# Optimization experiments

Hardware: AMD Instinct MI355X
Metric: run time of the kernel (lower is better)

## Reference

```python
import jax, jax.numpy as jnp
import numpy as np
from jax import lax

D_MODEL = 512
D_STATE = 16
D_CONV = 4
DT_RANK = 32  # ceil(512/16)


def setup_inputs() -> dict:
    key = jax.random.key(0)
    ks = jax.random.split(key, 8)
    B, L = 4, 2048
    x = jax.random.normal(ks[0], (B, L, D_MODEL), dtype=jnp.float32)
    A_log = jax.random.normal(ks[1], (D_MODEL, D_STATE), dtype=jnp.float32)
    D = jax.random.normal(ks[2], (D_MODEL,), dtype=jnp.float32)
    # torch Linear weight layout: (out_features, in_features)
    x_proj_w = jax.random.normal(ks[3], (DT_RANK + 2 * D_STATE, D_MODEL), dtype=jnp.float32) * (1.0 / np.sqrt(D_MODEL))
    dt_proj_w = jax.random.normal(ks[4], (D_MODEL, DT_RANK), dtype=jnp.float32) * (1.0 / np.sqrt(DT_RANK))
    dt_proj_b = jax.random.normal(ks[5], (D_MODEL,), dtype=jnp.float32) * 0.1
    # depthwise conv: (out_channels, in_channels/groups=1, kernel)
    conv_w = jax.random.normal(ks[6], (D_MODEL, 1, D_CONV), dtype=jnp.float32) * (1.0 / np.sqrt(D_CONV))
    conv_b = jax.random.normal(ks[7], (D_MODEL,), dtype=jnp.float32) * 0.1
    return {"x": x, "A_log": A_log, "D": D, "x_proj_w": x_proj_w,
            "dt_proj_w": dt_proj_w, "dt_proj_b": dt_proj_b,
            "conv_w": conv_w, "conv_b": conv_b}


def reference(x, A_log, D, x_proj_w, dt_proj_w, dt_proj_b, conv_w, conv_b):
    B, L, d_model = x.shape
    # causal depthwise conv1d: torch pads (d_conv-1) both sides then trims right -> left-pad only
    x_t = jnp.transpose(x, (0, 2, 1))  # (B, d, L)
    xc = lax.conv_general_dilated(
        x_t, conv_w, window_strides=(1,), padding=[(D_CONV - 1, 0)],
        feature_group_count=d_model)
    xc = xc + conv_b[None, :, None]
    xc = jnp.transpose(xc, (0, 2, 1))  # (B, L, d)

    x_dbl = xc @ x_proj_w.T  # (B, L, dt_rank + 2*d_state)
    dt = x_dbl[..., :DT_RANK]
    Bm = x_dbl[..., DT_RANK:DT_RANK + D_STATE]       # (B, L, n)
    C = x_dbl[..., DT_RANK + D_STATE:]               # (B, L, n)

    dt = jax.nn.softplus(dt @ dt_proj_w.T + dt_proj_b)  # (B, L, d)
    A = -jnp.exp(A_log.astype(jnp.float32))             # (d, n)
    dA = jnp.exp(jnp.einsum('bld,dn->bldn', dt, A))     # (B, L, d, n)
    dBx = jnp.einsum('bld,bln->bldn', dt * xc, Bm)      # (B, L, d, n)

    def step(h, inputs):
        dA_t, dBx_t, C_t = inputs  # (B,d,n), (B,d,n), (B,n)
        h = dA_t * h + dBx_t
        y_t = jnp.einsum('bdn,bn->bd', h, C_t)
        return h, y_t

    h0 = jnp.zeros((B, d_model, D_STATE), dtype=x.dtype)
    _, ys = lax.scan(step, h0, (jnp.moveaxis(dA, 1, 0), jnp.moveaxis(dBx, 1, 0), jnp.moveaxis(C, 1, 0)))
    y = jnp.moveaxis(ys, 0, 1)  # (B, L, d)
    return y + xc * D[None, None, :]
```

## Files before the change

kernel.cpp:

```cpp
#include <hip/hip_runtime.h>
#include <stdint.h>

#define L_SEQ   2048
#define NBATCH  4
#define DM      512
#define DS      16
#define DR      32
#define NBDN    32768
#define NCH     64
#define CL      32
#define LOG2E   1.4426950408889634f

#define WS_DX    0
#define WS_XDBL  4194304
#define WS_WXT   4718592
#define WS_WDTT  4751360
#define WS_A2    4767744
#define WS_DTSUM 4775936
#define WS_S     4907008

__device__ __forceinline__ uint32_t bf16_rne_hi(float v) {
    uint32_t u = __float_as_uint(v);
    u += 0x7FFF + ((u >> 16) & 1);
    return u & 0xFFFF0000u;
}
__device__ __forceinline__ float bf_lo(uint32_t u) { return __uint_as_float(u << 16); }
__device__ __forceinline__ float bf_hi(uint32_t u) { return __uint_as_float(u & 0xFFFF0000u); }

__global__ void __launch_bounds__(256) k_prep(
        const float* __restrict__ Wx, const float* __restrict__ Wdt,
        const float* __restrict__ A_log, float* __restrict__ WxT,
        float* __restrict__ WdtT, float* __restrict__ A2) {
    int idx = blockIdx.x * 256 + threadIdx.x;
    if (idx < DM * 64) {
        int dd = idx >> 6, j = idx & 63;
        WxT[idx] = Wx[j * DM + dd];
    }
    if (idx < DR * DM) {
        int r = idx >> 9, dd = idx & 511;
        WdtT[idx] = Wdt[dd * DR + r];
    }
    if (idx < DM * DS)
        A2[idx] = -__expf(A_log[idx]) * LOG2E;
}

__global__ void __launch_bounds__(256) k_front(
        const float* __restrict__ x, const float* __restrict__ convw,
        const float* __restrict__ convb, const float* __restrict__ WxT,
        const float* __restrict__ WdtT, const float* __restrict__ dtb,
        uint32_t* __restrict__ dx, float* __restrict__ xdbl) {
    __shared__ float xcs[8][512];
    __shared__ float pt[8][8][64];
    __shared__ float xds[8][64];
    int t  = threadIdx.x;
    int r0 = blockIdx.x * 8;
    int b  = r0 >> 11, l0 = r0 & (L_SEQ - 1);
    int dq = t & 127, half = t >> 7;

    {
        const float4* wp = (const float4*)convw;
        float4 w0 = wp[dq * 4 + 0], w1 = wp[dq * 4 + 1];
        float4 w2 = wp[dq * 4 + 2], w3 = wp[dq * 4 + 3];
        float4 bias = ((const float4*)convb)[dq];
        #pragma unroll
        for (int i = 0; i < 4; ++i) {
            int row = half * 4 + i;
            int l   = l0 + row;
            const float* xr = x + ((size_t)(b * L_SEQ + l)) * DM + dq * 4;
            float4 acc = bias;
            float4 xv = *(const float4*)xr;
            acc.x = fmaf(xv.x, w0.w, acc.x); acc.y = fmaf(xv.y, w1.w, acc.y);
            acc.z = fmaf(xv.z, w2.w, acc.z); acc.w = fmaf(xv.w, w3.w, acc.w);
            if (l >= 1) {
                xv = *(const float4*)(xr - DM);
                acc.x = fmaf(xv.x, w0.z, acc.x); acc.y = fmaf(xv.y, w1.z, acc.y);
                acc.z = fmaf(xv.z, w2.z, acc.z); acc.w = fmaf(xv.w, w3.z, acc.w);
            }
            if (l >= 2) {
                xv = *(const float4*)(xr - 2 * DM);
                acc.x = fmaf(xv.x, w0.y, acc.x); acc.y = fmaf(xv.y, w1.y, acc.y);
                acc.z = fmaf(xv.z, w2.y, acc.z); acc.w = fmaf(xv.w, w3.y, acc.w);
            }
            if (l >= 3) {
                xv = *(const float4*)(xr - 3 * DM);
                acc.x = fmaf(xv.x, w0.x, acc.x); acc.y = fmaf(xv.y, w1.x, acc.y);
                acc.z = fmaf(xv.z, w2.x, acc.z); acc.w = fmaf(xv.w, w3.x, acc.w);
            }
            *(float4*)(&xcs[row][dq * 4]) = acc;
        }
    }
    __syncthreads();

    {
        int ks = t >> 5;
        int jp = t & 31;
        int k0 = ks * 64;
        float accA[8], accB[8];
        #pragma unroll
        for (int ri = 0; ri < 8; ++ri) { accA[ri] = 0.f; accB[ri] = 0.f; }
        const float2* wp2 = (const float2*)WxT;
        for (int k4 = 0; k4 < 16; ++k4) {
            float4 xr[8];
            #pragma unroll
            for (int ri = 0; ri < 8; ++ri)
                xr[ri] = *(const float4*)(&xcs[ri][k0 + k4 * 4]);
            #pragma unroll
            for (int kk = 0; kk < 4; ++kk) {
                float2 w2 = wp2[(size_t)(k0 + k4 * 4 + kk) * 32 + jp];
                #pragma unroll
                for (int ri = 0; ri < 8; ++ri) {
                    float xv = ((const float*)&xr[ri])[kk];
                    accA[ri] = fmaf(xv, w2.x, accA[ri]);
                    accB[ri] = fmaf(xv, w2.y, accB[ri]);
                }
            }
        }
        #pragma unroll
        for (int ri = 0; ri < 8; ++ri)
            *(float2*)(&pt[ks][ri][jp * 2]) = make_float2(accA[ri], accB[ri]);
    }
    __syncthreads();

    #pragma unroll
    for (int o = t; o < 512; o += 256) {
        int row = o >> 6, j2 = o & 63;
        float s = ((pt[0][row][j2] + pt[1][row][j2]) + (pt[2][row][j2] + pt[3][row][j2]))
                + ((pt[4][row][j2] + pt[5][row][j2]) + (pt[6][row][j2] + pt[7][row][j2]));
        xds[row][j2] = s;
        xdbl[(size_t)(r0 + row) * 64 + j2] = s;
    }
    __syncthreads();

    {
        float4 bias = ((const float4*)dtb)[dq];
        float4 z0 = bias, z1 = bias, z2 = bias, z3 = bias;
        for (int r = 0; r < DR; ++r) {
            float4 w4 = *(const float4*)(WdtT + r * DM + dq * 4);
            float x0 = xds[half * 4 + 0][r];
            float x1 = xds[half * 4 + 1][r];
            float x2 = xds[half * 4 + 2][r];
            float x3 = xds[half * 4 + 3][r];
            z0.x = fmaf(x0, w4.x, z0.x); z0.y = fmaf(x0, w4.y, z0.y);
            z0.z = fmaf(x0, w4.z, z0.z); z0.w = fmaf(x0, w4.w, z0.w);
            z1.x = fmaf(x1, w4.x, z1.x); z1.y = fmaf(x1, w4.y, z1.y);
            z1.z = fmaf(x1, w4.z, z1.z); z1.w = fmaf(x1, w4.w, z1.w);
            z2.x = fmaf(x2, w4.x, z2.x); z2.y = fmaf(x2, w4.y, z2.y);
            z2.z = fmaf(x2, w4.z, z2.z); z2.w = fmaf(x2, w4.w, z2.w);
            z3.x = fmaf(x3, w4.x, z3.x); z3.y = fmaf(x3, w4.y, z3.y);
            z3.z = fmaf(x3, w4.z, z3.z); z3.w = fmaf(x3, w4.w, z3.w);
        }
        float4 zz[4] = {z0, z1, z2, z3};
        #pragma unroll
        for (int i = 0; i < 4; ++i) {
            int row = half * 4 + i;
            float4 zi = zz[i];
            float4 sp;
            sp.x = fmaxf(zi.x, 0.f) + log1pf(__expf(-fabsf(zi.x)));
            sp.y = fmaxf(zi.y, 0.f) + log1pf(__expf(-fabsf(zi.y)));
            sp.z = fmaxf(zi.z, 0.f) + log1pf(__expf(-fabsf(zi.z)));
            sp.w = fmaxf(zi.w, 0.f) + log1pf(__expf(-fabsf(zi.w)));
            uint4 pk;
            pk.x = bf16_rne_hi(sp.x) | (bf16_rne_hi(xcs[row][dq * 4 + 0]) >> 16);
            pk.y = bf16_rne_hi(sp.y) | (bf16_rne_hi(xcs[row][dq * 4 + 1]) >> 16);
            pk.z = bf16_rne_hi(sp.z) | (bf16_rne_hi(xcs[row][dq * 4 + 2]) >> 16);
            pk.w = bf16_rne_hi(sp.w) | (bf16_rne_hi(xcs[row][dq * 4 + 3]) >> 16);
            *(uint4*)(dx + ((size_t)(b * L_SEQ + l0 + row)) * DM + dq * 4) = pk;
        }
    }
}

__global__ void __launch_bounds__(256) k_scan1(
        const uint32_t* __restrict__ dx, const float* __restrict__ xdbl,
        const float* __restrict__ A2, float* __restrict__ S,
        float* __restrict__ dtsum) {
    int t      = threadIdx.x;
    int lane   = t & 63;
    int wv     = t >> 6;
    int dlocal = lane & 15;
    int nq     = lane >> 4;
    int db8    = blockIdx.x & 7;
    int c      = blockIdx.x >> 3;
    int b      = blockIdx.y;
    int d      = (db8 * 4 + wv) * 16 + dlocal;
    int l0     = c * CL;

    float4 a2 = *(const float4*)(A2 + (size_t)d * DS + nq * 4);
    float h0 = 0.f, h1 = 0.f, h2 = 0.f, h3 = 0.f;
    float dsum = 0.f;
    const uint32_t* dxp = dx + ((size_t)(b * L_SEQ + l0)) * DM + d;
    const float*    bp  = xdbl + ((size_t)(b * L_SEQ + l0)) * 64 + DR + nq * 4;

    #pragma unroll 8
    for (int i = 0; i < CL; ++i) {
        uint32_t v = dxp[(size_t)i * DM];
        float dt = bf_hi(v);
        float xv = bf_lo(v);
        float4 B4 = *(const float4*)(bp + (size_t)i * 64);
        float uu = dt * xv;
        dsum += dt;
        float dA;
        dA = exp2f(dt * a2.x); h0 = fmaf(dA, h0, uu * B4.x);
        dA = exp2f(dt * a2.y); h1 = fmaf(dA, h1, uu * B4.y);
        dA = exp2f(dt * a2.z); h2 = fmaf(dA, h2, uu * B4.z);
        dA = exp2f(dt * a2.w); h3 = fmaf(dA, h3, uu * B4.w);
    }
    float4 sv; sv.x = h0; sv.y = h1; sv.z = h2; sv.w = h3;
    *(float4*)(S + (size_t)c * NBDN + ((size_t)(b * DM + d)) * DS + nq * 4) = sv;
    if (nq == 0)
        dtsum[c * (NBATCH * DM) + b * DM + d] = dsum;
}

__global__ void __launch_bounds__(256) k_scan2(
        const float* __restrict__ dtsum, const float* __restrict__ A2,
        float* __restrict__ S) {
    int t  = blockIdx.x * 256 + threadIdx.x;
    float a2 = A2[t & (DM * DS - 1)];
    int bd = t >> 4;
    float H = 0.f;
    #pragma unroll 8
    for (int cc = 0; cc < NCH; ++cc) {
        float p = exp2f(a2 * dtsum[cc * (NBATCH * DM) + bd]);
        float s = S[(size_t)cc * NBDN + t];
        S[(size_t)cc * NBDN + t] = H;
        H = fmaf(p, H, s);
    }
}

__global__ void __launch_bounds__(256) k_scan3(
        const uint32_t* __restrict__ dx, const float* __restrict__ xdbl,
        const float* __restrict__ A2, const float* __restrict__ Dvec,
        const float* __restrict__ Hin, float* __restrict__ out) {
    int t      = threadIdx.x;
    int lane   = t & 63;
    int wv     = t >> 6;
    int dlocal = lane & 15;
    int nq     = lane >> 4;
    int db8    = blockIdx.x & 7;
    int c      = blockIdx.x >> 3;
    int b      = blockIdx.y;
    int d      = (db8 * 4 + wv) * 16 + dlocal;
    int l0     = c * CL;

    float4 a2 = *(const float4*)(A2 + (size_t)d * DS + nq * 4);
    float Dv = Dvec[d];
    float4 hv = *(const float4*)(Hin + (size_t)c * NBDN + ((size_t)(b * DM + d)) * DS + nq * 4);
    float h0 = hv.x, h1 = hv.y, h2 = hv.z, h3 = hv.w;

    const uint32_t* dxp = dx + ((size_t)(b * L_SEQ + l0)) * DM + d;
    const float*    bp  = xdbl + ((size_t)(b * L_SEQ + l0)) * 64 + DR + nq * 4;
    float* op = out + ((size_t)(b * L_SEQ + l0)) * DM + d;

    #pragma unroll 8
    for (int i = 0; i < CL; ++i) {
        uint32_t v = dxp[(size_t)i * DM];
        float dt = bf_hi(v);
        float xv = bf_lo(v);
        float4 B4 = *(const float4*)(bp + (size_t)i * 64);
        float4 C4 = *(const float4*)(bp + (size_t)i * 64 + DS);
        float uu = dt * xv;
        float dA;
        dA = exp2f(dt * a2.x); h0 = fmaf(dA, h0, uu * B4.x);
        dA = exp2f(dt * a2.y); h1 = fmaf(dA, h1, uu * B4.y);
        dA = exp2f(dt * a2.z); h2 = fmaf(dA, h2, uu * B4.z);
        dA = exp2f(dt * a2.w); h3 = fmaf(dA, h3, uu * B4.w);
        float p = fmaf(h3, C4.w, fmaf(h2, C4.z, fmaf(h1, C4.y, h0 * C4.x)));
        p += __shfl_xor(p, 16);
        p += __shfl_xor(p, 32);
        if (nq == 0) op[(size_t)i * DM] = fmaf(xv, Dv, p);
    }
}

extern "C" void kernel_launch(void* const* d_in, const int* in_sizes, int n_in,
                              void* d_out, int out_size, void* d_ws, size_t ws_size,
                              hipStream_t stream) {
    const float* x      = (const float*)d_in[0];
    const float* A_log  = (const float*)d_in[1];
    const float* Dvec   = (const float*)d_in[2];
    const float* Wx     = (const float*)d_in[3];
    const float* Wdt    = (const float*)d_in[4];
    const float* dtb    = (const float*)d_in[5];
    const float* convw  = (const float*)d_in[6];
    const float* convb  = (const float*)d_in[7];
    float* out = (float*)d_out;
    float* wsf = (float*)d_ws;

    uint32_t* dx    = (uint32_t*)(wsf + WS_DX);
    float*    xdbl  = wsf + WS_XDBL;
    float*    WxT   = wsf + WS_WXT;
    float*    WdtT  = wsf + WS_WDTT;
    float*    A2    = wsf + WS_A2;
    float*    dtsum = wsf + WS_DTSUM;
    float*    S     = wsf + WS_S;

    k_prep<<<128, 256, 0, stream>>>(Wx, Wdt, A_log, WxT, WdtT, A2);
    k_front<<<1024, 256, 0, stream>>>(x, convw, convb, WxT, WdtT, dtb, dx, xdbl);
    k_scan1<<<dim3(512, 4), 256, 0, stream>>>(dx, xdbl, A2, S, dtsum);
    k_scan2<<<128, 256, 0, stream>>>(dtsum, A2, S);
    k_scan3<<<dim3(512, 4), 256, 0, stream>>>(dx, xdbl, A2, Dvec, S, out);
}
```

Before: 100.9 us.

## Fuse chunk-local scan pass into front kernel and halve chunk length

Folds the first scan pass (per-chunk state and dt-sum) into the front projection kernel. The packed dt/x values and the B coefficients are reused from shared memory instead of being re-read from global memory, and one launch disappears. Chunk length drops from 32 to 16, which doubles the chunk count. That roughly halves the front grid, raises register pressure (16-row accumulators and 32 scan states per thread), and lengthens the serial loop in the second scan pass.

```diff
diff --git a/kernel.cpp b/kernel.cpp
--- a/kernel.cpp
+++ b/kernel.cpp
@@ -7,8 +7,8 @@
 #define DS      16
 #define DR      32
 #define NBDN    32768
-#define NCH     64
-#define CL      32
+#define NCH     128
+#define CL      16
 #define LOG2E   1.4426950408889634f
 
 #define WS_DX    0
@@ -17,7 +17,7 @@
 #define WS_WDTT  4751360
 #define WS_A2    4767744
 #define WS_DTSUM 4775936
-#define WS_S     4907008
+#define WS_S     5038080
 
 __device__ __forceinline__ uint32_t bf16_rne_hi(float v) {
     uint32_t u = __float_as_uint(v);
@@ -48,14 +48,20 @@
         const float* __restrict__ x, const float* __restrict__ convw,
         const float* __restrict__ convb, const float* __restrict__ WxT,
         const float* __restrict__ WdtT, const float* __restrict__ dtb,
-        uint32_t* __restrict__ dx, float* __restrict__ xdbl) {
-    __shared__ float xcs[8][512];
-    __shared__ float pt[8][8][64];
-    __shared__ float xds[8][64];
+        const float* __restrict__ A2,
+        uint32_t* __restrict__ dx, float* __restrict__ xdbl,
+        float* __restrict__ S, float* __restrict__ dtsum) {
+    __shared__ float xcs[CL][512];
+    __shared__ float pt[8][CL][64];
+    __shared__ float xds[CL][64];
+    uint32_t* xcs_u32 = (uint32_t*)&xcs[0][0];
+
     int t  = threadIdx.x;
-    int r0 = blockIdx.x * 8;
-    int b  = r0 >> 11, l0 = r0 & (L_SEQ - 1);
-    int dq = t & 127, half = t >> 7;
+    int c  = blockIdx.x;
+    int b  = blockIdx.y;
+    int l0 = c * CL;
+    int r0 = b * L_SEQ + l0;
+    int dq = t & 127, rg = t >> 7;
 
     {
         const float4* wp = (const float4*)convw;
@@ -63,8 +69,8 @@
         float4 w2 = wp[dq * 4 + 2], w3 = wp[dq * 4 + 3];
         float4 bias = ((const float4*)convb)[dq];
         #pragma unroll
-        for (int i = 0; i < 4; ++i) {
-            int row = half * 4 + i;
+        for (int i = 0; i < 8; ++i) {
+            int row = rg * 8 + i;
             int l   = l0 + row;
             const float* xr = x + ((size_t)(b * L_SEQ + l)) * DM + dq * 4;
             float4 acc = bias;
@@ -95,20 +101,20 @@
         int ks = t >> 5;
         int jp = t & 31;
         int k0 = ks * 64;
-        float accA[8], accB[8];
-        #pragma unroll
-        for (int ri = 0; ri < 8; ++ri) { accA[ri] = 0.f; accB[ri] = 0.f; }
+        float accA[CL], accB[CL];
+        #pragma unroll
+        for (int ri = 0; ri < CL; ++ri) { accA[ri] = 0.f; accB[ri] = 0.f; }
         const float2* wp2 = (const float2*)WxT;
         for (int k4 = 0; k4 < 16; ++k4) {
-            float4 xr[8];
-            #pragma unroll
-            for (int ri = 0; ri < 8; ++ri)
+            float4 xr[CL];
+            #pragma unroll
+            for (int ri = 0; ri < CL; ++ri)
                 xr[ri] = *(const float4*)(&xcs[ri][k0 + k4 * 4]);
             #pragma unroll
             for (int kk = 0; kk < 4; ++kk) {
                 float2 w2 = wp2[(size_t)(k0 + k4 * 4 + kk) * 32 + jp];
                 #pragma unroll
-                for (int ri = 0; ri < 8; ++ri) {
+                for (int ri = 0; ri < CL; ++ri) {
                     float xv = ((const float*)&xr[ri])[kk];
                     accA[ri] = fmaf(xv, w2.x, accA[ri]);
                     accB[ri] = fmaf(xv, w2.y, accB[ri]);
@@ -116,13 +122,13 @@
             }
         }
         #pragma unroll
-        for (int ri = 0; ri < 8; ++ri)
+        for (int ri = 0; ri < CL; ++ri)
             *(float2*)(&pt[ks][ri][jp * 2]) = make_float2(accA[ri], accB[ri]);
     }
     __syncthreads();
 
     #pragma unroll
-    for (int o = t; o < 512; o += 256) {
+    for (int o = t; o < CL * 64; o += 256) {
         int row = o >> 6, j2 = o & 63;
         float s = ((pt[0][row][j2] + pt[1][row][j2]) + (pt[2][row][j2] + pt[3][row][j2]))
                 + ((pt[4][row][j2] + pt[5][row][j2]) + (pt[6][row][j2] + pt[7][row][j2]));
@@ -133,27 +139,22 @@
 
     {
         float4 bias = ((const float4*)dtb)[dq];
-        float4 z0 = bias, z1 = bias, z2 = bias, z3 = bias;
+        float4 z[8];
+        #pragma unroll
+        for (int i = 0; i < 8; ++i) z[i] = bias;
         for (int r = 0; r < DR; ++r) {
             float4 w4 = *(const float4*)(WdtT + r * DM + dq * 4);
-            float x0 = xds[half * 4 + 0][r];
-            float x1 = xds[half * 4 + 1][r];
-            float x2 = xds[half * 4 + 2][r];
-            float x3 = xds[half * 4 + 3][r];
-            z0.x = fmaf(x0, w4.x, z0.x); z0.y = fmaf(x0, w4.y, z0.y);
-            z0.z = fmaf(x0, w4.z, z0.z); z0.w = fmaf(x0, w4.w, z0.w);
-            z1.x = fmaf(x1, w4.x, z1.x); z1.y = fmaf(x1, w4.y, z1.y);
-            z1.z = fmaf(x1, w4.z, z1.z); z1.w = fmaf(x1, w4.w, z1.w);
-            z2.x = fmaf(x2, w4.x, z2.x); z2.y = fmaf(x2, w4.y, z2.y);
-            z2.z = fmaf(x2, w4.z, z2.z); z2.w = fmaf(x2, w4.w, z2.w);
-            z3.x = fmaf(x3, w4.x, z3.x); z3.y = fmaf(x3, w4.y, z3.y);
-            z3.z = fmaf(x3, w4.z, z3.z); z3.w = fmaf(x3, w4.w, z3.w);
-        }
-        float4 zz[4] = {z0, z1, z2, z3};
-        #pragma unroll
-        for (int i = 0; i < 4; ++i) {
-            int row = half * 4 + i;
-            float4 zi = zz[i];
+            #pragma unroll
+            for (int i = 0; i < 8; ++i) {
+                float xv = xds[rg * 8 + i][r];
+                z[i].x = fmaf(xv, w4.x, z[i].x); z[i].y = fmaf(xv, w4.y, z[i].y);
+                z[i].z = fmaf(xv, w4.z, z[i].z); z[i].w = fmaf(xv, w4.w, z[i].w);
+            }
+        }
+        #pragma unroll
+        for (int i = 0; i < 8; ++i) {
+            int row = rg * 8 + i;
+            float4 zi = z[i];
             float4 sp;
             sp.x = fmaxf(zi.x, 0.f) + log1pf(__expf(-fabsf(zi.x)));
             sp.y = fmaxf(zi.y, 0.f) + log1pf(__expf(-fabsf(zi.y)));
@@ -164,50 +165,61 @@
             pk.y = bf16_rne_hi(sp.y) | (bf16_rne_hi(xcs[row][dq * 4 + 1]) >> 16);
             pk.z = bf16_rne_hi(sp.z) | (bf16_rne_hi(xcs[row][dq * 4 + 2]) >> 16);
             pk.w = bf16_rne_hi(sp.w) | (bf16_rne_hi(xcs[row][dq * 4 + 3]) >> 16);
-            *(uint4*)(dx + ((size_t)(b * L_SEQ + l0 + row)) * DM + dq * 4) = pk;
-        }
-    }
-}
-
-__global__ void __launch_bounds__(256) k_scan1(
-        const uint32_t* __restrict__ dx, const float* __restrict__ xdbl,
-        const float* __restrict__ A2, float* __restrict__ S,
-        float* __restrict__ dtsum) {
-    int t      = threadIdx.x;
-    int lane   = t & 63;
-    int wv     = t >> 6;
-    int dlocal = lane & 15;
-    int nq     = lane >> 4;
-    int db8    = blockIdx.x & 7;
-    int c      = blockIdx.x >> 3;
-    int b      = blockIdx.y;
-    int d      = (db8 * 4 + wv) * 16 + dlocal;
-    int l0     = c * CL;
-
-    float4 a2 = *(const float4*)(A2 + (size_t)d * DS + nq * 4);
-    float h0 = 0.f, h1 = 0.f, h2 = 0.f, h3 = 0.f;
-    float dsum = 0.f;
-    const uint32_t* dxp = dx + ((size_t)(b * L_SEQ + l0)) * DM + d;
-    const float*    bp  = xdbl + ((size_t)(b * L_SEQ + l0)) * 64 + DR + nq * 4;
-
-    #pragma unroll 8
-    for (int i = 0; i < CL; ++i) {
-        uint32_t v = dxp[(size_t)i * DM];
-        float dt = bf_hi(v);
-        float xv = bf_lo(v);
-        float4 B4 = *(const float4*)(bp + (size_t)i * 64);
-        float uu = dt * xv;
-        dsum += dt;
-        float dA;
-        dA = exp2f(dt * a2.x); h0 = fmaf(dA, h0, uu * B4.x);
-        dA = exp2f(dt * a2.y); h1 = fmaf(dA, h1, uu * B4.y);
-        dA = exp2f(dt * a2.z); h2 = fmaf(dA, h2, uu * B4.z);
-        dA = exp2f(dt * a2.w); h3 = fmaf(dA, h3, uu * B4.w);
-    }
-    float4 sv; sv.x = h0; sv.y = h1; sv.z = h2; sv.w = h3;
-    *(float4*)(S + (size_t)c * NBDN + ((size_t)(b * DM + d)) * DS + nq * 4) = sv;
-    if (nq == 0)
-        dtsum[c * (NBATCH * DM) + b * DM + d] = dsum;
+            *(uint4*)(dx + ((size_t)(r0 + row)) * DM + dq * 4) = pk;
+            *(uint4*)(&xcs_u32[row * 512 + dq * 4]) = pk;
+        }
+    }
+    __syncthreads();
+
+    {
+        int d0 = t * 2;
+        float a2a[DS], a2b[DS];
+        {
+            const float4* apA = (const float4*)(A2 + (size_t)d0 * DS);
+            const float4* apB = (const float4*)(A2 + (size_t)(d0 + 1) * DS);
+            #pragma unroll
+            for (int q = 0; q < 4; ++q) {
+                float4 va = apA[q], vb = apB[q];
+                a2a[q*4+0] = va.x; a2a[q*4+1] = va.y; a2a[q*4+2] = va.z; a2a[q*4+3] = va.w;
+                a2b[q*4+0] = vb.x; a2b[q*4+1] = vb.y; a2b[q*4+2] = vb.z; a2b[q*4+3] = vb.w;
+            }
+        }
+        float hA[DS], hB[DS];
+        #pragma unroll
+        for (int n = 0; n < DS; ++n) { hA[n] = 0.f; hB[n] = 0.f; }
+        float dsA = 0.f, dsB = 0.f;
+
+        for (int i = 0; i < CL; ++i) {
+            uint2 w2 = *(const uint2*)(&xcs_u32[i * 512 + d0]);
+            float dtA = bf_hi(w2.x), xvA = bf_lo(w2.x);
+            float dtB = bf_hi(w2.y), xvB = bf_lo(w2.y);
+            float uA = dtA * xvA, uB = dtB * xvB;
+            dsA += dtA; dsB += dtB;
+            #pragma unroll
+            for (int q = 0; q < 4; ++q) {
+                float4 B4 = *(const float4*)(&xds[i][DR + q * 4]);
+                float Bs[4] = {B4.x, B4.y, B4.z, B4.w};
+                #pragma unroll
+                for (int k = 0; k < 4; ++k) {
+                    int n = q * 4 + k;
+                    float dA;
+                    dA = exp2f(dtA * a2a[n]); hA[n] = fmaf(dA, hA[n], uA * Bs[k]);
+                    dA = exp2f(dtB * a2b[n]); hB[n] = fmaf(dA, hB[n], uB * Bs[k]);
+                }
+            }
+        }
+
+        size_t sbase = (size_t)c * NBDN + ((size_t)(b * DM + d0)) * DS;
+        float4* SpA = (float4*)(S + sbase);
+        float4* SpB = (float4*)(S + sbase + DS);
+        #pragma unroll
+        for (int q = 0; q < 4; ++q) {
+            SpA[q] = make_float4(hA[q*4+0], hA[q*4+1], hA[q*4+2], hA[q*4+3]);
+            SpB[q] = make_float4(hB[q*4+0], hB[q*4+1], hB[q*4+2], hB[q*4+3]);
+        }
+        dtsum[c * (NBATCH * DM) + b * DM + d0]     = dsA;
+        dtsum[c * (NBATCH * DM) + b * DM + d0 + 1] = dsB;
+    }
 }
 
 __global__ void __launch_bounds__(256) k_scan2(
@@ -293,8 +305,8 @@
     float*    S     = wsf + WS_S;
 
     k_prep<<<128, 256, 0, stream>>>(Wx, Wdt, A_log, WxT, WdtT, A2);
-    k_front<<<1024, 256, 0, stream>>>(x, convw, convb, WxT, WdtT, dtb, dx, xdbl);
-    k_scan1<<<dim3(512, 4), 256, 0, stream>>>(dx, xdbl, A2, S, dtsum);
+    k_front<<<dim3(NCH, NBATCH), 256, 0, stream>>>(x, convw, convb, WxT, WdtT, dtb,
+                                                   A2, dx, xdbl, S, dtsum);
     k_scan2<<<128, 256, 0, stream>>>(dtsum, A2, S);
-    k_scan3<<<dim3(512, 4), 256, 0, stream>>>(dx, xdbl, A2, Dvec, S, out);
-}
+    k_scan3<<<dim3(8 * NCH, NBATCH), 256, 0, stream>>>(dx, xdbl, A2, Dvec, S, out);
+}
```

Result: no change. 101.1 us (+0.1%).
